# Kernel optimization log

Measured on AMD Instinct MI355X. Metric: run time of the kernel, lower is better.

The kernel has to match this reference:

```python
import jax, jax.numpy as jnp
import numpy as np

WS = 7        # window_size
SHIFT = 3     # shift_size
HEADS = 6
DIM = 192
HIDDEN = DIM * 6  # mlp_ratio=6
EPS = 1e-5


def _rel_pos_index(ws):
    # static relative-position index, (ws*ws, ws*ws) int
    coords = np.stack(np.meshgrid(np.arange(ws), np.arange(ws), indexing='ij')).reshape(2, -1)
    rel = coords[:, :, None] - coords[:, None, :]            # (2, N, N)
    rel = rel.transpose(1, 2, 0)                             # (N, N, 2)
    rel[:, :, 0] += ws - 1
    rel[:, :, 1] += ws - 1
    rel[:, :, 0] *= 2 * ws - 1
    return rel.sum(-1)


def _layernorm(t, g, b):
    m = t.mean(-1, keepdims=True)
    v = jnp.mean((t - m) ** 2, axis=-1, keepdims=True)
    return (t - m) * jax.lax.rsqrt(v + EPS) * g + b


def setup_inputs() -> dict:
    key = jax.random.key(0)
    ks = jax.random.split(key, 8)
    B, H, W = 16, 56, 56
    x = jax.random.normal(ks[0], (B, H * W, DIM), dtype=jnp.float32)
    p = lambda k, s: (jax.random.normal(k, s, dtype=jnp.float32) * 0.02)
    return {
        'x': x, 'H': H, 'W': W,
        'ln1_g': jnp.ones((DIM,), jnp.float32), 'ln1_b': jnp.zeros((DIM,), jnp.float32),
        'qkv_w': p(ks[1], (3 * DIM, DIM)), 'qkv_b': jnp.zeros((3 * DIM,), jnp.float32),
        'rpb': p(ks[2], ((2 * WS - 1) ** 2, HEADS)),
        'proj_w': p(ks[3], (DIM, DIM)), 'proj_b': jnp.zeros((DIM,), jnp.float32),
        'ln2_g': jnp.ones((DIM,), jnp.float32), 'ln2_b': jnp.zeros((DIM,), jnp.float32),
        'fc1_w': p(ks[4], (HIDDEN, DIM)), 'fc1_b': jnp.zeros((HIDDEN,), jnp.float32),
        'fc2_w': p(ks[5], (DIM, HIDDEN)), 'fc2_b': jnp.zeros((DIM,), jnp.float32),
    }


def reference(x, H, W, ln1_g, ln1_b, qkv_w, qkv_b, rpb, proj_w, proj_b,
              ln2_g, ln2_b, fc1_w, fc1_b, fc2_w, fc2_b):
    B, L, C = x.shape
    hd = C // HEADS
    shortcut = x
    h = _layernorm(x, ln1_g, ln1_b).reshape(B, H, W, C)
    pad_r = (WS - W % WS) % WS
    pad_b = (WS - H % WS) % WS
    h = jnp.pad(h, ((0, 0), (0, pad_b), (0, pad_r), (0, 0)))
    Hp, Wp = H + pad_b, W + pad_r
    if SHIFT > 0:
        h = jnp.roll(h, (-SHIFT, -SHIFT), axis=(1, 2))
    # window partition -> (nW*B, WS*WS, C)
    h = h.reshape(B, Hp // WS, WS, Wp // WS, WS, C).transpose(0, 1, 3, 2, 4, 5)
    h = h.reshape(-1, WS * WS, C)
    nB, N, _ = h.shape
    qkv = (h @ qkv_w.T + qkv_b).reshape(nB, N, 3, HEADS, hd).transpose(2, 0, 3, 1, 4)
    q, k, v = qkv[0], qkv[1], qkv[2]       # (nB, heads, N, hd)
    scale = hd ** -0.5
    attn = jnp.einsum('bhnd,bhmd->bhnm', q * scale, k)
    idx = _rel_pos_index(WS)
    bias = rpb[idx.reshape(-1)].reshape(N, N, HEADS).transpose(2, 0, 1)  # (heads, N, N)
    attn = jax.nn.softmax(attn + bias[None], axis=-1)
    out = jnp.einsum('bhnm,bhmd->bhnd', attn, v).transpose(0, 2, 1, 3).reshape(nB, N, C)
    out = out @ proj_w.T + proj_b
    # window reverse -> (B, Hp, Wp, C)
    out = out.reshape(B, Hp // WS, Wp // WS, WS, WS, C).transpose(0, 1, 3, 2, 4, 5)
    out = out.reshape(B, Hp, Wp, C)
    if SHIFT > 0:
        out = jnp.roll(out, (SHIFT, SHIFT), axis=(1, 2))
    out = out[:, :H, :W, :].reshape(B, H * W, C)
    x = shortcut + out
    h2 = _layernorm(x, ln2_g, ln2_b)
    h2 = jax.nn.gelu(h2 @ fc1_w.T + fc1_b, approximate=False)
    return x + (h2 @ fc2_w.T + fc2_b)
```

## Files before the change

### kernel.cpp

```cpp
#include <hip/hip_runtime.h>

typedef unsigned short u16;
typedef __bf16 bf16x8 __attribute__((ext_vector_type(8)));
typedef __bf16 bf16x2_t __attribute__((ext_vector_type(2)));
typedef float f32x4 __attribute__((ext_vector_type(4)));

#define AS1 __attribute__((address_space(1)))
#define AS3 __attribute__((address_space(3)))

__device__ __forceinline__ void gld16(const void* g, void* l) {
  __builtin_amdgcn_global_load_lds((const AS1 void*)g, (AS3 void*)l, 16, 0, 0);
}

__device__ __forceinline__ u16 f2bf(float f) {
  union { float f; unsigned int u; } v; v.f = f;
  unsigned int u = v.u;
  u += 0x7fffu + ((u >> 16) & 1u);
  return (u16)(u >> 16);
}
__device__ __forceinline__ float bf2f(u16 h) {
  union { unsigned int u; float f; } v; v.u = ((unsigned int)h) << 16; return v.f;
}
__device__ __forceinline__ unsigned int pk2(float a, float b) {
#if __has_builtin(__builtin_amdgcn_cvt_pk_bf16_f32)
  union { bf16x2_t v; unsigned int u; } c;
  c.v = __builtin_amdgcn_cvt_pk_bf16_f32(a, b);
  return c.u;
#else
  return (unsigned int)f2bf(a) | ((unsigned int)f2bf(b) << 16);
#endif
}
__device__ __forceinline__ float gelu_f(float v) {
  float u = v * (1.5957691216f + 0.0713548163f * v * v);
  return v * __builtin_amdgcn_rcpf(1.0f + __expf(-u));
}

__global__ __launch_bounds__(256) void cast_weights(
    const float* __restrict__ w0, const float* __restrict__ w1,
    const float* __restrict__ w2, const float* __restrict__ w3,
    u16* __restrict__ o0, u16* __restrict__ o1,
    u16* __restrict__ o2, u16* __restrict__ o3) {
  int i = blockIdx.x * 256 + threadIdx.x;
  if (i < 110592) o0[i] = f2bf(w0[i]);
  if (i < 36864) {
    int n = i / 192, kp = i - n * 192;
    int h = kp >> 5, dp = kp & 31;
    int d = (dp & 1) ? ((dp >> 1) + 16) : (dp >> 1);
    o1[i] = f2bf(w1[n * 192 + h * 32 + d]);
  }
  if (i < 221184) o2[i] = f2bf(w2[i]);
  if (i < 221184) o3[i] = f2bf(w3[i]);
}

__global__ __launch_bounds__(256) void build_btab(
    const float* __restrict__ rpb, float* __restrict__ btab) {
  int id = blockIdx.x * 256 + threadIdx.x;
  int head = id >> 12;
  int m = (id >> 6) & 63;
  int r = id & 63;
  float v;
  if (m >= 49) v = -1e30f;
  else if (r >= 49) v = 0.0f;
  else {
    int mi = m / 7, mj = m - mi * 7;
    int ri = r / 7, rj = r - ri * 7;
    v = rpb[((ri - mi + 6) * 13 + (rj - mj + 6)) * 6 + head];
  }
  btab[id] = v;
}

__global__ __launch_bounds__(256) void ln_kernel(
    const float* __restrict__ x, const float* __restrict__ g,
    const float* __restrict__ b, u16* __restrict__ out) {
  int row = blockIdx.x * 4 + (threadIdx.x >> 6);
  int lane = threadIdx.x & 63;
  const float* xr = x + (long)row * 192;
  float e0 = xr[lane], e1 = xr[lane + 64], e2 = xr[lane + 128];
  float s = e0 + e1 + e2;
  #pragma unroll
  for (int o = 1; o < 64; o <<= 1) s += __shfl_xor(s, o);
  float mean = s * (1.0f / 192.0f);
  float d0 = e0 - mean, d1 = e1 - mean, d2 = e2 - mean;
  float q = d0 * d0 + d1 * d1 + d2 * d2;
  #pragma unroll
  for (int o = 1; o < 64; o <<= 1) q += __shfl_xor(q, o);
  float rstd = rsqrtf(q * (1.0f / 192.0f) + 1e-5f);
  u16* orow = out + (long)row * 192;
  orow[lane]       = f2bf(d0 * rstd * g[lane]       + b[lane]);
  orow[lane + 64]  = f2bf(d1 * rstd * g[lane + 64]  + b[lane + 64]);
  orow[lane + 128] = f2bf(d2 * rstd * g[lane + 128] + b[lane + 128]);
}

template<int MODE>
__global__ __launch_bounds__(256, 3) void gemm_kernel(
    const u16* __restrict__ A, const u16* __restrict__ W,
    const float* __restrict__ bias, const float* __restrict__ resid,
    void* __restrict__ out, int N, int K) {
  constexpr int TT = 20;
  constexpr int BUF = TT * 512;
  __shared__ u16 lds[2 * BUF];
  float* ct = (float*)lds;
  const int tid = threadIdx.x;
  const int wave = tid >> 6, lane = tid & 63;
  const int wm = wave >> 1, wn = wave & 1;
  const int quad = lane >> 4, l15 = lane & 15;
  const long bm = (long)blockIdx.x * 128;
  const int bn = blockIdx.y * 192;
  const int NC = K >> 5;

  for (int t = wave; t < TT; t += 4) {
    const u16* g = (t < 8)
        ? (A + (bm + t * 16 + l15) * (long)K + quad * 8)
        : (W + (long)(bn + (t - 8) * 16 + l15) * K + quad * 8);
    gld16(g, &lds[t * 512]);
  }
  __syncthreads();

  f32x4 acc[4][6] = {};
  for (int c = 0; c < NC; c++) {
    const int cur = c & 1;
    if (c + 1 < NC) {
      const int kof = (c + 1) * 32 + quad * 8;
      u16* nb = &lds[(cur ^ 1) * BUF];
      for (int t = wave; t < TT; t += 4) {
        const u16* g = (t < 8)
            ? (A + (bm + t * 16 + l15) * (long)K + kof)
            : (W + (long)(bn + (t - 8) * 16 + l15) * K + kof);
        gld16(g, nb + t * 512);
      }
    }
    const u16* buf = lds + cur * BUF;
    bf16x8 af[4];
    #pragma unroll
    for (int mt = 0; mt < 4; mt++)
      af[mt] = *(const bf16x8*)&buf[(wm * 4 + mt) * 512 + lane * 8];
    #pragma unroll
    for (int nt = 0; nt < 6; nt++) {
      bf16x8 bfr = *(const bf16x8*)&buf[(8 + wn * 6 + nt) * 512 + lane * 8];
      #pragma unroll
      for (int mt = 0; mt < 4; mt++)
        acc[mt][nt] = __builtin_amdgcn_mfma_f32_16x16x32_bf16(af[mt], bfr, acc[mt][nt], 0, 0, 0);
    }
    __syncthreads();
  }

  #pragma unroll
  for (int h = 0; h < 2; h++) {
    #pragma unroll
    for (int g = 0; g < 2; g++) {
      if (wm == h && wn == g) {
        #pragma unroll
        for (int nt = 0; nt < 6; nt++) {
          int col = nt * 16 + l15;
          float bi = bias[bn + g * 96 + col];
          #pragma unroll
          for (int mt = 0; mt < 4; mt++) {
            int row0 = mt * 16 + quad * 4;
            #pragma unroll
            for (int j = 0; j < 4; j++)
              ct[(row0 + j) * 100 + col] = acc[mt][nt][j] + bi;
          }
        }
      }
      __syncthreads();
      #pragma unroll
      for (int it = 0; it < 6; it++) {
        int cc = it * 256 + tid;
        int row = cc / 24, i = cc - row * 24;
        float4 v = *(const float4*)&ct[row * 100 + i * 4];
        long idx = (bm + h * 64 + row) * (long)N + bn + g * 96 + i * 4;
        if (MODE == 2) {
          const float4 rv = *(const float4*)(resid + idx);
          v.x += rv.x; v.y += rv.y; v.z += rv.z; v.w += rv.w;
          *(float4*)((float*)out + idx) = v;
        } else {
          uint2 pk;
          pk.x = pk2(v.x, v.y);
          pk.y = pk2(v.z, v.w);
          *(uint2*)((u16*)out + idx) = pk;
        }
      }
      if (!(h == 1 && g == 1)) __syncthreads();
    }
  }
}

__global__ __launch_bounds__(256, 2) void mlp_kernel(
    const u16* __restrict__ hA, const u16* __restrict__ W1,
    const float* __restrict__ b1, const u16* __restrict__ W2,
    const float* __restrict__ b2, const float* __restrict__ resid,
    float* __restrict__ out) {
  __shared__ u16 wbuf[2 * 6144];
  __shared__ u16 hid[12800];
  __shared__ float sb1[1152];
  float* ct = (float*)hid;
  const int tid = threadIdx.x;
  const int wave = tid >> 6, lane = tid & 63;
  const int wm = wave >> 1, wn = wave & 1;
  const int quad = lane >> 4, l15 = lane & 15;
  const long bm = (long)blockIdx.x * 64;

  const long w1b = (long)(wave * 16 + l15) * 192 + quad * 8;
  const long w2b = (long)(wave * 16 + l15) * 1152 + quad * 8;
  const int dt0 = wave * 512, dt1 = (wave + 4) * 512, dt2 = (wave + 8) * 512;

  auto stageW1 = [&](int hc, int kc, int pb) {
    const u16* g = W1 + w1b + hc * 36864 + kc * 32;
    u16* d = wbuf + pb * 6144;
    gld16(g, d + dt0);
    gld16(g + 12288, d + dt1);
    gld16(g + 24576, d + dt2);
  };
  auto stageW2 = [&](int hc, int kc, int pb) {
    const u16* g = W2 + w2b + hc * 192 + kc * 32;
    u16* d = wbuf + pb * 6144;
    gld16(g, d + dt0);
    gld16(g + 73728, d + dt1);
    gld16(g + 147456, d + dt2);
  };

  stageW1(0, 0, 0);
  #pragma unroll
  for (int it = 0; it < 2; ++it) {
    int idx = it * 256 + tid;
    if (idx < 288) *(float4*)&sb1[idx * 4] = *(const float4*)&b1[idx * 4];
  }
  bf16x8 haf[2][6];
  #pragma unroll
  for (int mt = 0; mt < 2; mt++)
    #pragma unroll
    for (int kc = 0; kc < 6; kc++)
      haf[mt][kc] = *(const bf16x8*)&hA[(bm + wm * 32 + mt * 16 + l15) * 192 + kc * 32 + quad * 8];
  __syncthreads();

  f32x4 acc2[2][6] = {};
  for (int hc = 0; hc < 6; ++hc) {
    f32x4 acc1[6][2];
    #pragma unroll
    for (int nt = 0; nt < 6; nt++) {
      f32x4 bv = *(const f32x4*)&sb1[hc * 192 + wn * 96 + nt * 16 + quad * 4];
      acc1[nt][0] = bv;
      acc1[nt][1] = bv;
    }
    #pragma unroll
    for (int kc = 0; kc < 6; kc++) {
      if (kc < 5) stageW1(hc, kc + 1, (kc & 1) ^ 1);
      else        stageW2(hc, 0, (kc & 1) ^ 1);
      const u16* buf = wbuf + (kc & 1) * 6144;
      #pragma unroll
      for (int nt = 0; nt < 6; nt++) {
        bf16x8 wf = *(const bf16x8*)&buf[(wn * 6 + nt) * 512 + lane * 8];
        acc1[nt][0] = __builtin_amdgcn_mfma_f32_16x16x32_bf16(wf, haf[0][kc], acc1[nt][0], 0, 0, 0);
        acc1[nt][1] = __builtin_amdgcn_mfma_f32_16x16x32_bf16(wf, haf[1][kc], acc1[nt][1], 0, 0, 0);
      }
      __syncthreads();
    }
    #pragma unroll
    for (int nt = 0; nt < 6; nt++)
      #pragma unroll
      for (int mt = 0; mt < 2; mt++) {
        uint2 pk;
        pk.x = pk2(gelu_f(acc1[nt][mt][0]), gelu_f(acc1[nt][mt][1]));
        pk.y = pk2(gelu_f(acc1[nt][mt][2]), gelu_f(acc1[nt][mt][3]));
        *(uint2*)&hid[(wm * 32 + mt * 16 + l15) * 200 + wn * 96 + nt * 16 + quad * 4] = pk;
      }
    __syncthreads();
    #pragma unroll
    for (int kc = 0; kc < 6; kc++) {
      if (kc < 5)      stageW2(hc, kc + 1, (kc & 1) ^ 1);
      else if (hc < 5) stageW1(hc + 1, 0, (kc & 1) ^ 1);
      const u16* buf = wbuf + (kc & 1) * 6144;
      bf16x8 hf0 = *(const bf16x8*)&hid[(wm * 32 + l15) * 200 + kc * 32 + quad * 8];
      bf16x8 hf1 = *(const bf16x8*)&hid[(wm * 32 + 16 + l15) * 200 + kc * 32 + quad * 8];
      #pragma unroll
      for (int nt = 0; nt < 6; nt++) {
        bf16x8 wf = *(const bf16x8*)&buf[(wn * 6 + nt) * 512 + lane * 8];
        acc2[0][nt] = __builtin_amdgcn_mfma_f32_16x16x32_bf16(hf0, wf, acc2[0][nt], 0, 0, 0);
        acc2[1][nt] = __builtin_amdgcn_mfma_f32_16x16x32_bf16(hf1, wf, acc2[1][nt], 0, 0, 0);
      }
      __syncthreads();
    }
  }

  #pragma unroll
  for (int g = 0; g < 2; g++) {
    if (wn == g) {
      #pragma unroll
      for (int nt = 0; nt < 6; nt++) {
        int col = nt * 16 + l15;
        float bi = b2[g * 96 + col];
        #pragma unroll
        for (int mt = 0; mt < 2; mt++) {
          int row0 = wm * 32 + mt * 16 + quad * 4;
          #pragma unroll
          for (int j = 0; j < 4; j++)
            ct[(row0 + j) * 100 + col] = acc2[mt][nt][j] + bi;
        }
      }
    }
    __syncthreads();
    #pragma unroll
    for (int it = 0; it < 6; it++) {
      int cc = it * 256 + tid;
      int row = cc / 24, i = cc - row * 24;
      float4 v = *(const float4*)&ct[row * 100 + i * 4];
      long idx = (bm + row) * 192 + g * 96 + i * 4;
      const float4 rv = *(const float4*)(resid + idx);
      v.x += rv.x; v.y += rv.y; v.z += rv.z; v.w += rv.w;
      *(float4*)(out + idx) = v;
    }
    if (g == 0) __syncthreads();
  }
}

__global__ __launch_bounds__(256) void attn_kernel(
    const u16* __restrict__ qkv, const float* __restrict__ btab,
    u16* __restrict__ attn) {
  __shared__ u16 lds[4 * 7040];
  __shared__ float sbias[64 * 65];
  int tid = threadIdx.x;
  int wave = tid >> 6, lane = tid & 63;
  int quad = lane >> 4, l15 = lane & 15;
  int head = blockIdx.x % 6;
  int grp = blockIdx.x / 6;
  int win = grp * 4 + wave;
  int b = win >> 6, wy = (win >> 3) & 7, wx = win & 7;
  u16* lp = lds + wave * 7040;
  u16* lvt = lp + 4608;
  float* rsum = (float*)(lp + 6912);

  {
    const float* bsrc = btab + head * 4096;
    #pragma unroll
    for (int i = 0; i < 4; i++) {
      int idx4 = tid + i * 256;
      float4 v = *(const float4*)(bsrc + idx4 * 4);
      float* dst = &sbias[(idx4 >> 4) * 65 + (idx4 & 15) * 4];
      dst[0] = v.x; dst[1] = v.y; dst[2] = v.z; dst[3] = v.w;
    }
  }

  bf16x8 qb[4], ka[4];
  #pragma unroll
  for (int t = 0; t < 4; t++) {
    int n = t * 16 + l15;
    uint4 qv = {0, 0, 0, 0}, kv = {0, 0, 0, 0}, vv = {0, 0, 0, 0};
    if (n < 49) {
      int i = n / 7, j = n - i * 7;
      int y = wy * 7 + i + 3;  if (y >= 56) y -= 56;
      int xx = wx * 7 + j + 3; if (xx >= 56) xx -= 56;
      long base = ((long)(b * 3136 + y * 56 + xx)) * 576 + head * 32 + quad * 8;
      qv = *(const uint4*)(qkv + base);
      kv = *(const uint4*)(qkv + base + 192);
      vv = *(const uint4*)(qkv + base + 384);
    }
    qb[t] = *(const bf16x8*)&qv;
    ka[t] = *(const bf16x8*)&kv;
    const u16* vp = (const u16*)&vv;
    #pragma unroll
    for (int d = 0; d < 8; d++) lvt[(quad * 8 + d) * 72 + n] = vp[d];
  }

  f32x4 s[4][4];
  const f32x4 fz = {0.0f, 0.0f, 0.0f, 0.0f};
  #pragma unroll
  for (int tm = 0; tm < 4; tm++)
    #pragma unroll
    for (int tr = 0; tr < 4; tr++)
      s[tm][tr] = __builtin_amdgcn_mfma_f32_16x16x32_bf16(ka[tm], qb[tr], fz, 0, 0, 0);

  __syncthreads();

  const float scale = 0.17677669529663687f;
  float mx[4] = {-1e30f, -1e30f, -1e30f, -1e30f};
  #pragma unroll
  for (int tm = 0; tm < 4; tm++) {
    int m0 = tm * 16 + quad * 4;
    #pragma unroll
    for (int tr = 0; tr < 4; tr++) {
      int r = tr * 16 + l15;
      #pragma unroll
      for (int j = 0; j < 4; j++) {
        float v = s[tm][tr][j] * scale + sbias[(m0 + j) * 65 + r];
        s[tm][tr][j] = v;
        mx[tr] = fmaxf(mx[tr], v);
      }
    }
  }
  #pragma unroll
  for (int tr = 0; tr < 4; tr++) {
    mx[tr] = fmaxf(mx[tr], __shfl_xor(mx[tr], 16));
    mx[tr] = fmaxf(mx[tr], __shfl_xor(mx[tr], 32));
  }
  float sm[4] = {0.f, 0.f, 0.f, 0.f};
  #pragma unroll
  for (int tm = 0; tm < 4; tm++) {
    #pragma unroll
    for (int tr = 0; tr < 4; tr++) {
      int r = tr * 16 + l15;
      float e0 = __expf(s[tm][tr][0] - mx[tr]);
      float e1 = __expf(s[tm][tr][1] - mx[tr]);
      float e2 = __expf(s[tm][tr][2] - mx[tr]);
      float e3 = __expf(s[tm][tr][3] - mx[tr]);
      sm[tr] += (e0 + e1) + (e2 + e3);
      uint2 pk;
      pk.x = pk2(e0, e1);
      pk.y = pk2(e2, e3);
      *(uint2*)&lp[r * 72 + tm * 16 + quad * 4] = pk;
    }
  }
  #pragma unroll
  for (int tr = 0; tr < 4; tr++) {
    sm[tr] += __shfl_xor(sm[tr], 16);
    sm[tr] += __shfl_xor(sm[tr], 32);
  }
  if (quad == 0) {
    #pragma unroll
    for (int tr = 0; tr < 4; tr++) rsum[tr * 16 + l15] = __builtin_amdgcn_rcpf(sm[tr]);
  }

  f32x4 o[4][2] = {};
  #pragma unroll
  for (int ks = 0; ks < 2; ks++) {
    bf16x8 vb0 = *(const bf16x8*)&lvt[(l15) * 72 + ks * 32 + quad * 8];
    bf16x8 vb1 = *(const bf16x8*)&lvt[(16 + l15) * 72 + ks * 32 + quad * 8];
    #pragma unroll
    for (int rt = 0; rt < 4; rt++) {
      bf16x8 pf = *(const bf16x8*)&lp[(rt * 16 + l15) * 72 + ks * 32 + quad * 8];
      o[rt][0] = __builtin_amdgcn_mfma_f32_16x16x32_bf16(pf, vb0, o[rt][0], 0, 0, 0);
      o[rt][1] = __builtin_amdgcn_mfma_f32_16x16x32_bf16(pf, vb1, o[rt][1], 0, 0, 0);
    }
  }
  #pragma unroll
  for (int rt = 0; rt < 4; rt++) {
    #pragma unroll
    for (int j = 0; j < 4; j++) {
      int r = rt * 16 + quad * 4 + j;
      if (r < 49) {
        float inv = rsum[r];
        int i = r / 7, jj = r - i * 7;
        int y = wy * 7 + i + 3;   if (y >= 56) y -= 56;
        int xx = wx * 7 + jj + 3; if (xx >= 56) xx -= 56;
        long base = ((long)(b * 3136 + y * 56 + xx)) * 192 + head * 32 + 2 * l15;
        *(unsigned int*)&attn[base] = pk2(o[rt][0][j] * inv, o[rt][1][j] * inv);
      }
    }
  }
}

extern "C" void kernel_launch(void* const* d_in, const int* in_sizes, int n_in,
                              void* d_out, int out_size, void* d_ws, size_t ws_size,
                              hipStream_t stream) {
  (void)in_sizes; (void)n_in; (void)out_size; (void)ws_size;
  const float* x      = (const float*)d_in[0];
  const float* ln1_g  = (const float*)d_in[3];
  const float* ln1_b  = (const float*)d_in[4];
  const float* qkv_w  = (const float*)d_in[5];
  const float* qkv_b  = (const float*)d_in[6];
  const float* rpb    = (const float*)d_in[7];
  const float* proj_w = (const float*)d_in[8];
  const float* proj_b = (const float*)d_in[9];
  const float* ln2_g  = (const float*)d_in[10];
  const float* ln2_b  = (const float*)d_in[11];
  const float* fc1_w  = (const float*)d_in[12];
  const float* fc1_b  = (const float*)d_in[13];
  const float* fc2_w  = (const float*)d_in[14];
  const float* fc2_b  = (const float*)d_in[15];

  char* ws = (char*)d_ws;
  float* x2   = (float*)(ws + 0);
  u16* hA     = (u16*)(ws + 38535168);
  float* btab = (float*)(ws + 38535168);
  u16* qkv    = (u16*)(ws + 57802752);
  u16* attn   = (u16*)(ws + 115605504);
  u16* wbuf   = (u16*)(ws + 173408256);
  u16* qkv_wb  = wbuf;
  u16* proj_wb = wbuf + 110592;
  u16* fc1_wb  = wbuf + 147456;
  u16* fc2_wb  = wbuf + 368640;

  cast_weights<<<dim3(864), 256, 0, stream>>>(qkv_w, proj_w, fc1_w, fc2_w,
                                              qkv_wb, proj_wb, fc1_wb, fc2_wb);
  ln_kernel<<<dim3(12544), 256, 0, stream>>>(x, ln1_g, ln1_b, hA);
  gemm_kernel<0><<<dim3(392, 3), 256, 0, stream>>>(hA, qkv_wb, qkv_b, nullptr,
                                                   qkv, 576, 192);
  build_btab<<<dim3(96), 256, 0, stream>>>(rpb, btab);
  attn_kernel<<<dim3(1536), 256, 0, stream>>>(qkv, btab, attn);
  gemm_kernel<2><<<dim3(392, 1), 256, 0, stream>>>(attn, proj_wb, proj_b, x,
                                                   x2, 192, 192);
  ln_kernel<<<dim3(12544), 256, 0, stream>>>(x2, ln2_g, ln2_b, hA);
  mlp_kernel<<<dim3(784), 256, 0, stream>>>(hA, fc1_wb, fc1_b, fc2_wb, fc2_b,
                                            x2, (float*)d_out);
}
```

Before: 342.4 us.

## Load MLP weight fragments directly from global memory instead of LDS staging

The MLP kernel drops the double-buffered LDS staging of W1/W2 tiles through global_load_lds, along with the per-k-step barriers. Each wave now reads its bf16 weight fragments and the fc1 bias straight from global memory (expected to hit L2/cache). This removes the LDS traffic and barrier synchronisation and shrinks shared memory use, which may allow more resident blocks. In exchange, each pair of waves sharing a column group now issues its own redundant global loads, and there is no explicit prefetch to hide their latency.

```diff
diff --git a/kernel.cpp b/kernel.cpp
--- a/kernel.cpp
+++ b/kernel.cpp
@@ -190,9 +190,7 @@
     const float* __restrict__ b1, const u16* __restrict__ W2,
     const float* __restrict__ b2, const float* __restrict__ resid,
     float* __restrict__ out) {
-  __shared__ u16 wbuf[2 * 6144];
-  __shared__ u16 hid[12800];
-  __shared__ float sb1[1152];
+  __shared__ u16 hid[64 * 200];
   float* ct = (float*)hid;
   const int tid = threadIdx.x;
   const int wave = tid >> 6, lane = tid & 63;
@@ -200,60 +198,34 @@
   const int quad = lane >> 4, l15 = lane & 15;
   const long bm = (long)blockIdx.x * 64;
 
-  const long w1b = (long)(wave * 16 + l15) * 192 + quad * 8;
-  const long w2b = (long)(wave * 16 + l15) * 1152 + quad * 8;
-  const int dt0 = wave * 512, dt1 = (wave + 4) * 512, dt2 = (wave + 8) * 512;
-
-  auto stageW1 = [&](int hc, int kc, int pb) {
-    const u16* g = W1 + w1b + hc * 36864 + kc * 32;
-    u16* d = wbuf + pb * 6144;
-    gld16(g, d + dt0);
-    gld16(g + 12288, d + dt1);
-    gld16(g + 24576, d + dt2);
-  };
-  auto stageW2 = [&](int hc, int kc, int pb) {
-    const u16* g = W2 + w2b + hc * 192 + kc * 32;
-    u16* d = wbuf + pb * 6144;
-    gld16(g, d + dt0);
-    gld16(g + 73728, d + dt1);
-    gld16(g + 147456, d + dt2);
-  };
-
-  stageW1(0, 0, 0);
-  #pragma unroll
-  for (int it = 0; it < 2; ++it) {
-    int idx = it * 256 + tid;
-    if (idx < 288) *(float4*)&sb1[idx * 4] = *(const float4*)&b1[idx * 4];
-  }
   bf16x8 haf[2][6];
   #pragma unroll
   for (int mt = 0; mt < 2; mt++)
     #pragma unroll
     for (int kc = 0; kc < 6; kc++)
       haf[mt][kc] = *(const bf16x8*)&hA[(bm + wm * 32 + mt * 16 + l15) * 192 + kc * 32 + quad * 8];
-  __syncthreads();
+
+  const u16* pw1 = W1 + (long)(wn * 96 + l15) * 192 + quad * 8;
+  const u16* pw2 = W2 + (long)(wn * 96 + l15) * 1152 + quad * 8;
 
   f32x4 acc2[2][6] = {};
   for (int hc = 0; hc < 6; ++hc) {
     f32x4 acc1[6][2];
     #pragma unroll
     for (int nt = 0; nt < 6; nt++) {
-      f32x4 bv = *(const f32x4*)&sb1[hc * 192 + wn * 96 + nt * 16 + quad * 4];
+      f32x4 bv = *(const f32x4*)&b1[hc * 192 + wn * 96 + nt * 16 + quad * 4];
       acc1[nt][0] = bv;
       acc1[nt][1] = bv;
     }
+    const u16* w1h = pw1 + (long)hc * 36864;
     #pragma unroll
     for (int kc = 0; kc < 6; kc++) {
-      if (kc < 5) stageW1(hc, kc + 1, (kc & 1) ^ 1);
-      else        stageW2(hc, 0, (kc & 1) ^ 1);
-      const u16* buf = wbuf + (kc & 1) * 6144;
       #pragma unroll
       for (int nt = 0; nt < 6; nt++) {
-        bf16x8 wf = *(const bf16x8*)&buf[(wn * 6 + nt) * 512 + lane * 8];
+        bf16x8 wf = *(const bf16x8*)(w1h + nt * 3072 + kc * 32);
         acc1[nt][0] = __builtin_amdgcn_mfma_f32_16x16x32_bf16(wf, haf[0][kc], acc1[nt][0], 0, 0, 0);
         acc1[nt][1] = __builtin_amdgcn_mfma_f32_16x16x32_bf16(wf, haf[1][kc], acc1[nt][1], 0, 0, 0);
       }
-      __syncthreads();
     }
     #pragma unroll
     for (int nt = 0; nt < 6; nt++)
@@ -265,21 +237,19 @@
         *(uint2*)&hid[(wm * 32 + mt * 16 + l15) * 200 + wn * 96 + nt * 16 + quad * 4] = pk;
       }
     __syncthreads();
+    const u16* w2h = pw2 + hc * 192;
     #pragma unroll
     for (int kc = 0; kc < 6; kc++) {
-      if (kc < 5)      stageW2(hc, kc + 1, (kc & 1) ^ 1);
-      else if (hc < 5) stageW1(hc + 1, 0, (kc & 1) ^ 1);
-      const u16* buf = wbuf + (kc & 1) * 6144;
       bf16x8 hf0 = *(const bf16x8*)&hid[(wm * 32 + l15) * 200 + kc * 32 + quad * 8];
       bf16x8 hf1 = *(const bf16x8*)&hid[(wm * 32 + 16 + l15) * 200 + kc * 32 + quad * 8];
       #pragma unroll
       for (int nt = 0; nt < 6; nt++) {
-        bf16x8 wf = *(const bf16x8*)&buf[(wn * 6 + nt) * 512 + lane * 8];
+        bf16x8 wf = *(const bf16x8*)(w2h + nt * 18432 + kc * 32);
         acc2[0][nt] = __builtin_amdgcn_mfma_f32_16x16x32_bf16(hf0, wf, acc2[0][nt], 0, 0, 0);
         acc2[1][nt] = __builtin_amdgcn_mfma_f32_16x16x32_bf16(hf1, wf, acc2[1][nt], 0, 0, 0);
       }
-      __syncthreads();
-    }
+    }
+    __syncthreads();
   }
 
   #pragma unroll
```

New measurement: 432.6 us. 1.26x slower.
